# Performance work log

Hardware: AMD Instinct MI355X
Metric: run time of the kernel (lower is better)

Reference implementation:

```python
import jax, jax.numpy as jnp
import numpy as np

OUTPUT_LENGTH = 2048  # init_kwargs: output_length


def setup_inputs() -> dict:
    key = jax.random.key(0)
    k1, k2 = jax.random.split(key)
    B, N, C = 16, 512, 512
    encoder_output = jax.random.normal(k1, (B, N, C), dtype=jnp.float32)
    log_durations = jax.random.normal(k2, (B, N, 1), dtype=jnp.float32)
    return {"encoder_output": encoder_output, "log_durations": log_durations}


def _alignment(log_durations, max_length):
    # log_durations: (B, N, 1) -> durations (B, N), matching the numpy uint8 math:
    # dur = uint8(2^log + 1e-4) * (log > 0); uint8 cast truncates (values stay < 256 here).
    ld = log_durations[..., 0]                                   # (B, N)
    mask = (ld > 0)
    dur = (jnp.floor(jnp.power(2.0, ld) + 1e-4)).astype(jnp.int32) * mask.astype(jnp.int32)
    ends = jnp.cumsum(dur, axis=1)                               # (B, N) inclusive cumsum
    starts = ends - dur                                          # exclusive cumsum
    t = jnp.arange(max_length, dtype=jnp.int32)                  # (L,)
    # align[b, t, p] = 1 iff starts[b,p] <= t < ends[b,p]
    align = (t[None, :, None] >= starts[:, None, :]) & (t[None, :, None] < ends[:, None, :])
    return align.astype(jnp.float32)                             # (B, L, N)


def reference(encoder_output, log_durations):
    align = _alignment(log_durations, OUTPUT_LENGTH)             # (B, L, N)
    # (B, L, N) @ (B, N, C) -> (B, L, C)
    return jnp.einsum('bln,bnc->blc', align, encoder_output)
```

## Files before the change

### kernel.cpp

```cpp
#include <hip/hip_runtime.h>

#define B_SZ 16
#define N_SZ 512
#define C_SZ 512
#define L_SZ 2048
#define ROW4 (C_SZ / 4)
#define TOTAL4 (B_SZ * L_SZ * ROW4)

__global__ __launch_bounds__(N_SZ) void build_idx_kernel(
    const float* __restrict__ log_durations,
    int* __restrict__ idx)
{
    __shared__ int wsum[8];
    const int b    = blockIdx.x;
    const int n    = threadIdx.x;
    const int lane = n & 63;
    const int w    = n >> 6;

    const float ld = log_durations[b * N_SZ + n];
    int dur = 0;
    if (ld > 0.0f) dur = (int)floorf(exp2f(ld) + 1e-4f);

    int scan = dur;
    #pragma unroll
    for (int o = 1; o < 64; o <<= 1) {
        int v = __shfl_up(scan, o, 64);
        if (lane >= o) scan += v;
    }
    if (lane == 63) wsum[w] = scan;
    __syncthreads();

    int base = 0, total = 0;
    #pragma unroll
    for (int i = 0; i < 8; ++i) {
        const int s = wsum[i];
        if (i < w) base += s;
        total += s;
    }
    const int end   = base + scan;
    const int start = end - dur;

    if (start < L_SZ) {
        const int e = min(end, L_SZ);
        for (int t = start; t < e; ++t) idx[b * L_SZ + t] = n;
    }

    const int tmin = min(total, L_SZ);
    for (int t = tmin + n; t < L_SZ; t += N_SZ) idx[b * L_SZ + t] = -1;
}

#define G_BLOCKS 2048
#define G_THREADS 256
#define G_STRIDE (G_BLOCKS * G_THREADS)
#define G_ITERS (TOTAL4 / G_STRIDE)

__global__ __launch_bounds__(G_THREADS) void gather_kernel(
    const float4* __restrict__ enc,
    const int*    __restrict__ idx,
    float4*       __restrict__ out)
{
    const int g0 = blockIdx.x * G_THREADS + threadIdx.x;
    #pragma unroll
    for (int it = 0; it < G_ITERS; ++it) {
        const int g   = g0 + it * G_STRIDE;
        const int row = g >> 7;
        const int b   = row >> 11;
        const int c4  = g & (ROW4 - 1);
        const int p   = idx[row];
        float4 v = make_float4(0.f, 0.f, 0.f, 0.f);
        if (p >= 0) v = enc[(size_t)((b << 9) + p) * ROW4 + c4];
        out[g] = v;
    }
}

extern "C" void kernel_launch(void* const* d_in, const int* in_sizes, int n_in,
                              void* d_out, int out_size, void* d_ws, size_t ws_size,
                              hipStream_t stream) {
    const float* enc = (const float*)d_in[0];
    const float* ld  = (const float*)d_in[1];
    float* out       = (float*)d_out;
    int* idx         = (int*)d_ws;

    build_idx_kernel<<<B_SZ, N_SZ, 0, stream>>>(ld, idx);
    gather_kernel<<<G_BLOCKS, G_THREADS, 0, stream>>>(
        (const float4*)enc, idx, (float4*)out);
}
```

Baseline: 83.26 us.

## Fuse duration scan and gather into one kernel with per-block binary search

Drops the separate index-building kernel and its global idx buffer. Each block of the fused kernel recomputes the per-batch duration prefix sum in shared memory, binary-searches the source token for each of its 16 output rows, then gathers and writes those rows. This removes one kernel launch, the serialized per-token index writes and the idx round trip through memory. In exchange, every block redoes the 512-element scan, which is redundant compute added to a memory-bound copy.

Measured after the change: 86.73 us. 1.04x slower.

```diff
diff --git a/kernel.cpp b/kernel.cpp
--- a/kernel.cpp
+++ b/kernel.cpp
@@ -5,23 +5,32 @@
 #define C_SZ 512
 #define L_SZ 2048
 #define ROW4 (C_SZ / 4)
-#define TOTAL4 (B_SZ * L_SZ * ROW4)
+#define BLK_ROWS 16
+#define THREADS 256
+#define GRID (B_SZ * L_SZ / BLK_ROWS)
 
-__global__ __launch_bounds__(N_SZ) void build_idx_kernel(
-    const float* __restrict__ log_durations,
-    int* __restrict__ idx)
+__global__ __launch_bounds__(THREADS) void lenreg_fused_kernel(
+    const float4* __restrict__ enc,
+    const float*  __restrict__ ldur,
+    float4*       __restrict__ out)
 {
-    __shared__ int wsum[8];
-    const int b    = blockIdx.x;
-    const int n    = threadIdx.x;
-    const int lane = n & 63;
-    const int w    = n >> 6;
+    __shared__ int ends[N_SZ];
+    __shared__ int wsum[4];
+    __shared__ int rowp[BLK_ROWS];
 
-    const float ld = log_durations[b * N_SZ + n];
-    int dur = 0;
-    if (ld > 0.0f) dur = (int)floorf(exp2f(ld) + 1e-4f);
+    const int t    = threadIdx.x;
+    const int lane = t & 63;
+    const int w    = t >> 6;
+    const int b    = blockIdx.x >> 7;
+    const int l0   = (blockIdx.x & 127) << 4;
 
-    int scan = dur;
+    const int n0 = t * 2, n1 = n0 + 1;
+    const float f0 = ldur[b * N_SZ + n0];
+    const float f1 = ldur[b * N_SZ + n1];
+    const int d0 = (f0 > 0.f) ? (int)floorf(exp2f(f0) + 1e-4f) : 0;
+    const int d1 = (f1 > 0.f) ? (int)floorf(exp2f(f1) + 1e-4f) : 0;
+
+    int scan = d0 + d1;
     #pragma unroll
     for (int o = 1; o < 64; o <<= 1) {
         int v = __shfl_up(scan, o, 64);
@@ -29,47 +38,45 @@
     }
     if (lane == 63) wsum[w] = scan;
     __syncthreads();
-
     int base = 0, total = 0;
     #pragma unroll
-    for (int i = 0; i < 8; ++i) {
+    for (int i = 0; i < 4; ++i) {
         const int s = wsum[i];
         if (i < w) base += s;
         total += s;
     }
-    const int end   = base + scan;
-    const int start = end - dur;
+    const int incl1 = base + scan;
+    ends[n1] = incl1;
+    ends[n0] = incl1 - d1;
+    __syncthreads();
 
-    if (start < L_SZ) {
-        const int e = min(end, L_SZ);
-        for (int t = start; t < e; ++t) idx[b * L_SZ + t] = n;
+    if (t < BLK_ROWS) {
+        const int l = l0 + t;
+        int p = -1;
+        if (l < total) {
+            int lo = 0, hi = N_SZ;
+            #pragma unroll
+            for (int it = 0; it < 10; ++it) {
+                const int mid = (lo + hi) >> 1;
+                if (ends[mid] > l) hi = mid; else lo = mid + 1;
+            }
+            p = lo;
+        }
+        rowp[t] = p;
     }
+    __syncthreads();
 
-    const int tmin = min(total, L_SZ);
-    for (int t = tmin + n; t < L_SZ; t += N_SZ) idx[b * L_SZ + t] = -1;
-}
-
-#define G_BLOCKS 2048
-#define G_THREADS 256
-#define G_STRIDE (G_BLOCKS * G_THREADS)
-#define G_ITERS (TOTAL4 / G_STRIDE)
-
-__global__ __launch_bounds__(G_THREADS) void gather_kernel(
-    const float4* __restrict__ enc,
-    const int*    __restrict__ idx,
-    float4*       __restrict__ out)
-{
-    const int g0 = blockIdx.x * G_THREADS + threadIdx.x;
+    const size_t outBase = (size_t)(b * L_SZ + l0) * ROW4;
+    const int    encBase = b * N_SZ * ROW4;
     #pragma unroll
-    for (int it = 0; it < G_ITERS; ++it) {
-        const int g   = g0 + it * G_STRIDE;
-        const int row = g >> 7;
-        const int b   = row >> 11;
-        const int c4  = g & (ROW4 - 1);
-        const int p   = idx[row];
+    for (int i = 0; i < 8; ++i) {
+        const int e  = t + i * THREADS;
+        const int r  = e >> 7;
+        const int c4 = e & (ROW4 - 1);
+        const int p  = rowp[r];
         float4 v = make_float4(0.f, 0.f, 0.f, 0.f);
-        if (p >= 0) v = enc[(size_t)((b << 9) + p) * ROW4 + c4];
-        out[g] = v;
+        if (p >= 0) v = enc[encBase + p * ROW4 + c4];
+        out[outBase + e] = v;
     }
 }
 
@@ -79,9 +86,7 @@
     const float* enc = (const float*)d_in[0];
     const float* ld  = (const float*)d_in[1];
     float* out       = (float*)d_out;
-    int* idx         = (int*)d_ws;
 
-    build_idx_kernel<<<B_SZ, N_SZ, 0, stream>>>(ld, idx);
-    gather_kernel<<<G_BLOCKS, G_THREADS, 0, stream>>>(
-        (const float4*)enc, idx, (float4*)out);
+    lenreg_fused_kernel<<<GRID, THREADS, 0, stream>>>(
+        (const float4*)enc, ld, (float4*)out);
 }
```
